# Kernel tuning notes

Measured on AMD Instinct MI355X. Metric: run time of the kernel, lower is better.

Reference implementation:

```python
import jax, jax.numpy as jnp
import numpy as np

N_NODES = 100000
N_EDGES = 1600000
K = 10          # APPNP propagation steps
ALPHA = 0.1     # teleport probability


def appnp_propagate(src, dst, h):
    """DGL APPNPConv (eval mode, no edge dropout): symmetric-normalized
    k-step personalized-pagerank propagation over the edge list."""
    n = h.shape[0]
    deg = jax.ops.segment_sum(jnp.ones_like(dst, dtype=h.dtype), dst, num_segments=n)
    norm = jnp.clip(deg, 1.0, None) ** -0.5  # [N]
    h0 = h
    for _ in range(K):
        msg = (h * norm[:, None])[src]                      # [E, D] gather
        agg = jax.ops.segment_sum(msg, dst, num_segments=n) # [N, D] scatter-add
        h = (1.0 - ALPHA) * agg * norm[:, None] + ALPHA * h0
    return h


def setup_inputs() -> dict:
    key = jax.random.key(0)
    ks = jax.random.split(key, 7)
    input_dim, hidden, classes = 256, 48, 16
    features = jax.random.normal(ks[0], (N_NODES, input_dim), dtype=jnp.float32)
    src = jax.random.randint(ks[1], (N_EDGES,), 0, N_NODES, dtype=jnp.int32)
    dst = jax.random.randint(ks[2], (N_EDGES,), 0, N_NODES, dtype=jnp.int32)
    # xavier_normal-ish init for fc weights
    W1 = jax.random.normal(ks[3], (hidden, input_dim), dtype=jnp.float32) * (2.0 / (hidden + input_dim)) ** 0.5
    b1 = jnp.zeros((hidden,), dtype=jnp.float32)
    W2 = jax.random.normal(ks[4], (classes, hidden), dtype=jnp.float32) * (2.0 / (classes + hidden)) ** 0.5
    b2 = jnp.zeros((classes,), dtype=jnp.float32)
    return {"features": features, "src": src, "dst": dst,
            "W1": W1, "b1": b1, "W2": W2, "b2": b2}


def reference(features, src, dst, W1, b1, W2, b2):
    # fc1
    h = features @ W1.T + b1              # [N, hidden]
    # layer1: APPNP propagation
    x = appnp_propagate(src, dst, h)
    # fc2 + elu
    x = jax.nn.elu(x @ W2.T + b2)         # [N, classes]
    # layer2: APPNP propagation
    x = appnp_propagate(src, dst, x)
    return jax.nn.elu(x)
```

## Files before the change

### kernel.cpp

```cpp
#include <hip/hip_runtime.h>
#include <hip/hip_fp16.h>
#include <math.h>

#define IN_DIM 256
#define HID 48
#define CLS 16
#define K_STEPS 10
#define ALPHA 0.1f


__global__ void zero_int_kernel(int* __restrict__ p, int n) {
    int i = blockIdx.x * blockDim.x + threadIdx.x;
    if (i < n) p[i] = 0;
}

__global__ void hist_kernel(const int* __restrict__ dst, int* __restrict__ deg, int nE) {
    int i = blockIdx.x * blockDim.x + threadIdx.x;
    if (i < nE) atomicAdd(&deg[dst[i]], 1);
}

__global__ void norm_kernel(const int* __restrict__ deg, float* __restrict__ nrm, int n) {
    int i = blockIdx.x * blockDim.x + threadIdx.x;
    if (i < n) nrm[i] = rsqrtf(fmaxf((float)deg[i], 1.0f));
}


__global__ __launch_bounds__(256) void scan1_kernel(const int* __restrict__ deg,
                                                    int* __restrict__ bsum, int n) {
    __shared__ int ls[256];
    int t = threadIdx.x;
    int base = blockIdx.x * 1024 + t * 4;
    int s = 0;
    if (base + 3 < n) {
        int4 d = *(const int4*)(deg + base);
        s = d.x + d.y + d.z + d.w;
    } else {
        for (int i = 0; i < 4; i++) if (base + i < n) s += deg[base + i];
    }
    ls[t] = s; __syncthreads();
    for (int o = 128; o > 0; o >>= 1) {
        if (t < o) ls[t] += ls[t + o];
        __syncthreads();
    }
    if (t == 0) bsum[blockIdx.x] = ls[0];
}

__global__ void scan2_kernel(int* __restrict__ bsum, int* __restrict__ off, int nb, int n) {
    if (threadIdx.x == 0 && blockIdx.x == 0) {
        int run = 0;
        for (int i = 0; i < nb; i++) { int t = bsum[i]; bsum[i] = run; run += t; }
        off[n] = run;
    }
}

__global__ __launch_bounds__(256) void scan3_kernel(const int* __restrict__ deg,
                                                    const int* __restrict__ bsum,
                                                    int* __restrict__ off,
                                                    int* __restrict__ cursor, int n) {
    __shared__ int ts[256];
    int t = threadIdx.x;
    int base = blockIdx.x * 1024 + t * 4;
    int d0 = 0, d1 = 0, d2 = 0, d3 = 0;
    if (base + 3 < n) {
        int4 d = *(const int4*)(deg + base);
        d0 = d.x; d1 = d.y; d2 = d.z; d3 = d.w;
    } else {
        if (base     < n) d0 = deg[base];
        if (base + 1 < n) d1 = deg[base + 1];
        if (base + 2 < n) d2 = deg[base + 2];
        if (base + 3 < n) d3 = deg[base + 3];
    }
    int s = d0 + d1 + d2 + d3;
    ts[t] = s; __syncthreads();
    for (int o = 1; o < 256; o <<= 1) {
        int v = (t >= o) ? ts[t - o] : 0;
        __syncthreads();
        ts[t] += v;
        __syncthreads();
    }
    int ex = ts[t] - s + bsum[blockIdx.x];
    int p0 = ex, p1 = ex + d0, p2 = p1 + d1, p3 = p2 + d2;
    if (base     < n) { off[base]     = p0; cursor[base]     = p0; }
    if (base + 1 < n) { off[base + 1] = p1; cursor[base + 1] = p1; }
    if (base + 2 < n) { off[base + 2] = p2; cursor[base + 2] = p2; }
    if (base + 3 < n) { off[base + 3] = p3; cursor[base + 3] = p3; }
}


__global__ __launch_bounds__(256) void fill8_kernel(
    const int* __restrict__ src, const int* __restrict__ dst,
    int* __restrict__ cursor, int* __restrict__ csrc, int nE, int nper)
{
    const int g  = blockIdx.x & 7;
    const int bi = blockIdx.x >> 3;
    const int nb = gridDim.x >> 3;
    const int lo = g * nper, hi = lo + nper;
    for (int i = bi * 256 + threadIdx.x; i < nE; i += nb * 256) {
        int d = dst[i];
        if (d >= lo && d < hi) {
            int p = atomicAdd(&cursor[d], 1);
            csrc[p] = src[i];
        }
    }
}


__global__ __launch_bounds__(256) void wc_kernel(
    const float* __restrict__ W1, const float* __restrict__ W2,
    const float* __restrict__ b1, float* __restrict__ Wc, float* __restrict__ bc)
{
    int c = blockIdx.x;
    int k = threadIdx.x;
    float acc = 0.0f;
    #pragma unroll
    for (int j = 0; j < HID; j++)
        acc = fmaf(W2[c * HID + j], W1[j * IN_DIM + k], acc);
    Wc[c * IN_DIM + k] = acc;
    if (k == 0) {
        float b = 0.0f;
        for (int j = 0; j < HID; j++) b = fmaf(W2[c * HID + j], b1[j], b);
        bc[c] = b;
    }
}


#define BM 128
#define BK 16
__global__ __launch_bounds__(256) void fcz_kernel(
    const float* __restrict__ X, const float* __restrict__ Wc,
    const float* __restrict__ bc, const float* __restrict__ nrm,
    float* __restrict__ z0, __half* __restrict__ A, int n)
{
    __shared__ float Xs[BK][BM + 1];
    __shared__ float Ws[BK][CLS];
    const int t = threadIdx.x;
    const int tx = t & 31;
    const int ty = t >> 5;
    const int mbase = blockIdx.x * BM;
    float acc[4][2] = {{0}};

    for (int k0 = 0; k0 < IN_DIM; k0 += BK) {
        #pragma unroll
        for (int c0 = 0; c0 < 2; c0++) {
            int c = t + c0 * 256;
            int m = c >> 2, kc = (c & 3) << 2;
            int gm = mbase + m;
            float4 xv = make_float4(0.f, 0.f, 0.f, 0.f);
            if (gm < n) xv = *(const float4*)(X + (size_t)gm * IN_DIM + k0 + kc);
            Xs[kc + 0][m] = xv.x; Xs[kc + 1][m] = xv.y;
            Xs[kc + 2][m] = xv.z; Xs[kc + 3][m] = xv.w;
        }
        if (t < 64) {
            int j = t >> 2, kc = (t & 3) << 2;
            float4 wv = *(const float4*)(Wc + (size_t)j * IN_DIM + k0 + kc);
            Ws[kc + 0][j] = wv.x; Ws[kc + 1][j] = wv.y;
            Ws[kc + 2][j] = wv.z; Ws[kc + 3][j] = wv.w;
        }
        __syncthreads();
        #pragma unroll
        for (int k = 0; k < BK; k++) {
            float a[4], b[2];
            #pragma unroll
            for (int im = 0; im < 4; im++) a[im] = Xs[k][tx + 32 * im];
            #pragma unroll
            for (int jn = 0; jn < 2; jn++) b[jn] = Ws[k][ty * 2 + jn];
            #pragma unroll
            for (int im = 0; im < 4; im++)
                #pragma unroll
                for (int jn = 0; jn < 2; jn++)
                    acc[im][jn] = fmaf(a[im], b[jn], acc[im][jn]);
        }
        __syncthreads();
    }

    #pragma unroll
    for (int im = 0; im < 4; im++) {
        int m = mbase + tx + 32 * im;
        if (m < n) {
            float nv = nrm[m];
            float r0 = acc[im][0] + bc[ty * 2 + 0];
            float r1 = acc[im][1] + bc[ty * 2 + 1];
            size_t idx = (size_t)m * CLS + ty * 2;
            z0[idx] = r0;
            z0[idx + 1] = r1;
            ((__half2*)A)[(size_t)m * 8 + ty] = __floats2half2_rn(r0 * nv, r1 * nv);
        }
    }
}


struct __align__(8) half4 { __half2 a, b; };

__device__ __forceinline__ void hacc(float4& acc, half4 w) {
    float2 lo = __half22float2(w.a);
    float2 hi = __half22float2(w.b);
    acc.x += lo.x; acc.y += lo.y; acc.z += hi.x; acc.w += hi.y;
}
__device__ __forceinline__ float eluf(float x) {
    return x > 0.0f ? x : expm1f(x);
}

template<int MODE>
__global__ __launch_bounds__(256) void gatherh_kernel(
    const int* __restrict__ off, const int* __restrict__ csrc,
    const half4* __restrict__ A, const float4* __restrict__ tele,
    const float* __restrict__ nrm, const float4* __restrict__ b2v,
    half4* __restrict__ outp, float4* __restrict__ x0out,
    float4* __restrict__ outf, int n)
{
    const int v = blockIdx.x * 64 + threadIdx.y;
    if (v >= n) return;
    const int lane = threadIdx.x;

    const int s = off[v], e = off[v + 1];
    float4 a0 = make_float4(0.f, 0.f, 0.f, 0.f), a1 = a0;
    int i = s;
    for (; i < e && (i & 3); i++)
        hacc(a0, A[(size_t)csrc[i] * 4 + lane]);
    for (; i + 8 <= e; i += 8) {
        int4 u = *(const int4*)(csrc + i);
        int4 q = *(const int4*)(csrc + i + 4);
        half4 w0 = A[(size_t)u.x * 4 + lane];
        half4 w1 = A[(size_t)u.y * 4 + lane];
        half4 w2 = A[(size_t)u.z * 4 + lane];
        half4 w3 = A[(size_t)u.w * 4 + lane];
        half4 w4 = A[(size_t)q.x * 4 + lane];
        half4 w5 = A[(size_t)q.y * 4 + lane];
        half4 w6 = A[(size_t)q.z * 4 + lane];
        half4 w7 = A[(size_t)q.w * 4 + lane];
        hacc(a0, w0); hacc(a1, w1); hacc(a0, w2); hacc(a1, w3);
        hacc(a0, w4); hacc(a1, w5); hacc(a0, w6); hacc(a1, w7);
    }
    for (; i + 4 <= e; i += 4) {
        int4 u = *(const int4*)(csrc + i);
        half4 w0 = A[(size_t)u.x * 4 + lane];
        half4 w1 = A[(size_t)u.y * 4 + lane];
        half4 w2 = A[(size_t)u.z * 4 + lane];
        half4 w3 = A[(size_t)u.w * 4 + lane];
        hacc(a0, w0); hacc(a1, w1); hacc(a0, w2); hacc(a1, w3);
    }
    for (; i < e; i++) hacc(a0, A[(size_t)csrc[i] * 4 + lane]);
    a0.x += a1.x; a0.y += a1.y; a0.z += a1.z; a0.w += a1.w;

    float nv = nrm[v];
    size_t o = (size_t)v * 4 + lane;
    float4 hv = tele[o];
    float4 r;
    r.x = (1.0f - ALPHA) * a0.x * nv + ALPHA * hv.x;
    r.y = (1.0f - ALPHA) * a0.y * nv + ALPHA * hv.y;
    r.z = (1.0f - ALPHA) * a0.z * nv + ALPHA * hv.z;
    r.w = (1.0f - ALPHA) * a0.w * nv + ALPHA * hv.w;

    if (MODE == 0) {
        half4 w;
        w.a = __floats2half2_rn(r.x * nv, r.y * nv);
        w.b = __floats2half2_rn(r.z * nv, r.w * nv);
        outp[o] = w;
    } else if (MODE == 1) {
        float4 b = b2v[lane];
        float4 x;
        x.x = eluf(r.x + b.x); x.y = eluf(r.y + b.y);
        x.z = eluf(r.z + b.z); x.w = eluf(r.w + b.w);
        x0out[o] = x;
        half4 w;
        w.a = __floats2half2_rn(x.x * nv, x.y * nv);
        w.b = __floats2half2_rn(x.z * nv, x.w * nv);
        outp[o] = w;
    } else {
        outf[o] = make_float4(eluf(r.x), eluf(r.y), eluf(r.z), eluf(r.w));
    }
}


extern "C" void kernel_launch(void* const* d_in, const int* in_sizes, int n_in,
                              void* d_out, int out_size, void* d_ws, size_t ws_size,
                              hipStream_t stream)
{
    const float* features = (const float*)d_in[0];
    const int*   src      = (const int*)d_in[1];
    const int*   dst      = (const int*)d_in[2];
    const float* W1       = (const float*)d_in[3];
    const float* b1       = (const float*)d_in[4];
    const float* W2       = (const float*)d_in[5];
    const float* b2       = (const float*)d_in[6];
    float* out = (float*)d_out;

    const int n  = in_sizes[0] / IN_DIM;
    const int nE = in_sizes[1];

    float* ws   = (float*)d_ws;
    float* nrm  = ws;
    float* z0   = nrm + n;
    float* x0   = z0 + (size_t)CLS * n;
    float* Wc   = x0 + (size_t)CLS * n;
    float* bc   = Wc + CLS * IN_DIM;
    __half* PH  = (__half*)(bc + 16);
    __half* QH  = PH + (size_t)CLS * n;
    int*   deg    = (int*)(QH + (size_t)CLS * n);
    int*   off    = deg + n;
    int*   cursor = off + n + 4;
    int*   bsum   = cursor + n;
    int*   csrc   = bsum + 1024;

    const int B = 256;
    const int nb = (n + 1023) / 1024;
    const int nper = (n + 7) / 8;

    zero_int_kernel<<<(n + B - 1) / B, B, 0, stream>>>(deg, n);
    hist_kernel<<<(nE + B - 1) / B, B, 0, stream>>>(dst, deg, nE);
    norm_kernel<<<(n + B - 1) / B, B, 0, stream>>>(deg, nrm, n);
    scan1_kernel<<<nb, 256, 0, stream>>>(deg, bsum, n);
    scan2_kernel<<<1, 64, 0, stream>>>(bsum, off, nb, n);
    scan3_kernel<<<nb, 256, 0, stream>>>(deg, bsum, off, cursor, n);

    fill8_kernel<<<2048, 256, 0, stream>>>(src, dst, cursor, csrc, nE, nper);

    wc_kernel<<<CLS, 256, 0, stream>>>(W1, W2, b1, Wc, bc);
    fcz_kernel<<<(n + BM - 1) / BM, 256, 0, stream>>>(features, Wc, bc, nrm, z0, PH, n);

    dim3 gblk(4, 64);
    int ggrid = (n + 63) / 64;

    __half* pa = PH; __half* pb = QH;
    for (int k = 0; k < K_STEPS; k++) {
        if (k < K_STEPS - 1)
            gatherh_kernel<0><<<ggrid, gblk, 0, stream>>>(
                off, csrc, (const half4*)pa, (const float4*)z0, nrm,
                nullptr, (half4*)pb, nullptr, nullptr, n);
        else
            gatherh_kernel<1><<<ggrid, gblk, 0, stream>>>(
                off, csrc, (const half4*)pa, (const float4*)z0, nrm,
                (const float4*)b2, (half4*)pb, (float4*)x0, nullptr, n);
        __half* t = pa; pa = pb; pb = t;
    }

    for (int k = 0; k < K_STEPS; k++) {
        if (k < K_STEPS - 1)
            gatherh_kernel<0><<<ggrid, gblk, 0, stream>>>(
                off, csrc, (const half4*)pa, (const float4*)x0, nrm,
                nullptr, (half4*)pb, nullptr, nullptr, n);
        else
            gatherh_kernel<2><<<ggrid, gblk, 0, stream>>>(
                off, csrc, (const half4*)pa, (const float4*)x0, nrm,
                nullptr, nullptr, nullptr, (float4*)out, n);
        __half* t = pa; pa = pb; pb = t;
    }
}
```

Measured before the change: 554.9 us.

## Bucket edges by destination range before CSR fill to cut redundant passes

```diff
diff --git a/kernel.cpp b/kernel.cpp
--- a/kernel.cpp
+++ b/kernel.cpp
@@ -8,15 +8,12 @@
 #define K_STEPS 10
 #define ALPHA 0.1f
 
+#define NCH 1024
+
 
 __global__ void zero_int_kernel(int* __restrict__ p, int n) {
     int i = blockIdx.x * blockDim.x + threadIdx.x;
     if (i < n) p[i] = 0;
-}
-
-__global__ void hist_kernel(const int* __restrict__ dst, int* __restrict__ deg, int nE) {
-    int i = blockIdx.x * blockDim.x + threadIdx.x;
-    if (i < nE) atomicAdd(&deg[dst[i]], 1);
 }
 
 __global__ void norm_kernel(const int* __restrict__ deg, float* __restrict__ nrm, int n) {
@@ -87,20 +84,85 @@
 }
 
 
-__global__ __launch_bounds__(256) void fill8_kernel(
+__global__ __launch_bounds__(256) void count8_kernel(
+    const int* __restrict__ dst, int* __restrict__ mtx, int nE, int nper)
+{
+    __shared__ int cnt[8];
+    const int t = threadIdx.x;
+    if (t < 8) cnt[t] = 0;
+    __syncthreads();
+    int lo = (int)((long long)nE * blockIdx.x / NCH);
+    int hi = (int)((long long)nE * (blockIdx.x + 1) / NCH);
+    for (int i = lo + t; i < hi; i += 256)
+        atomicAdd(&cnt[dst[i] / nper], 1);
+    __syncthreads();
+    if (t < 8) mtx[t * NCH + blockIdx.x] = cnt[t];
+}
+
+__global__ __launch_bounds__(1024) void bscan8_kernel(int* __restrict__ mtx)
+{
+    __shared__ int ts[NCH];
+    __shared__ int btot[8];
+    __shared__ int bbase[8];
+    const int t = threadIdx.x;
+    for (int b = 0; b < 8; b++) {
+        int v = mtx[b * NCH + t];
+        ts[t] = v; __syncthreads();
+        for (int o = 1; o < NCH; o <<= 1) {
+            int u = (t >= o) ? ts[t - o] : 0;
+            __syncthreads();
+            ts[t] += u;
+            __syncthreads();
+        }
+        mtx[b * NCH + t] = ts[t] - v;
+        if (t == NCH - 1) btot[b] = ts[t];
+        __syncthreads();
+    }
+    if (t == 0) {
+        int run = 0;
+        for (int b = 0; b < 8; b++) { bbase[b] = run; run += btot[b]; }
+    }
+    __syncthreads();
+    for (int b = 0; b < 8; b++)
+        mtx[b * NCH + t] += bbase[b];
+}
+
+__global__ __launch_bounds__(256) void scatter8_kernel(
     const int* __restrict__ src, const int* __restrict__ dst,
-    int* __restrict__ cursor, int* __restrict__ csrc, int nE, int nper)
+    const int* __restrict__ mtx, int* __restrict__ deg,
+    int2* __restrict__ ebuf, int nE, int nper)
+{
+    __shared__ int cur[8];
+    const int t = threadIdx.x;
+    if (t < 8) cur[t] = mtx[t * NCH + blockIdx.x];
+    __syncthreads();
+    int lo = (int)((long long)nE * blockIdx.x / NCH);
+    int hi = (int)((long long)nE * (blockIdx.x + 1) / NCH);
+    for (int i = lo + t; i < hi; i += 256) {
+        int d = dst[i];
+        int s = src[i];
+        atomicAdd(&deg[d], 1);
+        int p = atomicAdd(&cur[d / nper], 1);
+        ebuf[p] = make_int2(d, s);
+    }
+}
+
+__global__ __launch_bounds__(256) void fill2_kernel(
+    const int2* __restrict__ ebuf, const int* __restrict__ mtx,
+    int* __restrict__ cursor, int* __restrict__ csrc, int nE)
 {
     const int g  = blockIdx.x & 7;
-    const int bi = blockIdx.x >> 3;
-    const int nb = gridDim.x >> 3;
-    const int lo = g * nper, hi = lo + nper;
-    for (int i = bi * 256 + threadIdx.x; i < nE; i += nb * 256) {
-        int d = dst[i];
-        if (d >= lo && d < hi) {
-            int p = atomicAdd(&cursor[d], 1);
-            csrc[p] = src[i];
-        }
+    const int j  = blockIdx.x >> 3;
+    const int nbj = gridDim.x >> 3;
+    int bstart = mtx[g * NCH];
+    int bend   = (g < 7) ? mtx[(g + 1) * NCH] : nE;
+    long long len = bend - bstart;
+    int lo = bstart + (int)(len * j / nbj);
+    int hi = bstart + (int)(len * (j + 1) / nbj);
+    for (int i = lo + threadIdx.x; i < hi; i += 256) {
+        int2 e = ebuf[i];
+        int p = atomicAdd(&cursor[e.x], 1);
+        csrc[p] = e.y;
     }
 }
 
@@ -301,19 +363,22 @@
     int*   cursor = off + n + 4;
     int*   bsum   = cursor + n;
     int*   csrc   = bsum + 1024;
+    int*   mtx    = csrc + nE;
+    int2*  ebuf   = (int2*)z0;
 
     const int B = 256;
     const int nb = (n + 1023) / 1024;
     const int nper = (n + 7) / 8;
 
     zero_int_kernel<<<(n + B - 1) / B, B, 0, stream>>>(deg, n);
-    hist_kernel<<<(nE + B - 1) / B, B, 0, stream>>>(dst, deg, nE);
+    count8_kernel<<<NCH, 256, 0, stream>>>(dst, mtx, nE, nper);
+    bscan8_kernel<<<1, NCH, 0, stream>>>(mtx);
+    scatter8_kernel<<<NCH, 256, 0, stream>>>(src, dst, mtx, deg, ebuf, nE, nper);
     norm_kernel<<<(n + B - 1) / B, B, 0, stream>>>(deg, nrm, n);
     scan1_kernel<<<nb, 256, 0, stream>>>(deg, bsum, n);
     scan2_kernel<<<1, 64, 0, stream>>>(bsum, off, nb, n);
     scan3_kernel<<<nb, 256, 0, stream>>>(deg, bsum, off, cursor, n);
-
-    fill8_kernel<<<2048, 256, 0, stream>>>(src, dst, cursor, csrc, nE, nper);
+    fill2_kernel<<<2048, 256, 0, stream>>>(ebuf, mtx, cursor, csrc, nE);
 
     wc_kernel<<<CLS, 256, 0, stream>>>(W1, W2, b1, Wc, bc);
     fcz_kernel<<<(n + BM - 1) / BM, 256, 0, stream>>>(features, Wc, bc, nrm, z0, PH, n);
```

Measured after the change: 573.0 us. +3.3%, slower.
